# Kernel tuning notes

Measured on AMD Instinct MI355X. Metric: run time of the kernel, lower is better.

Reference implementation:

```python
import jax, jax.numpy as jnp
import numpy as np

L, T, B, D = 4, 512, 32, 1024
EPS = 1e-5


def _ln(x, g, b):
    # LayerNorm over last dim (torch nn.LayerNorm default eps=1e-5)
    m = jnp.mean(x, axis=-1, keepdims=True)
    v = jnp.var(x, axis=-1, keepdims=True)
    return (x - m) * jax.lax.rsqrt(v + EPS) * g + b


def setup_inputs() -> dict:
    key = jax.random.key(0)
    ks = jax.random.split(key, 6)
    s = np.float32(1.0 / np.sqrt(D))
    return {
        "x": jax.random.normal(ks[0], (T, B, D), dtype=jnp.float32),
        "state": jnp.zeros((L, B, D), dtype=jnp.float32),
        # per-layer gated-cell params (cell_cls(d_model, d_model))
        "Wf": jax.random.normal(ks[1], (L, D, D), dtype=jnp.float32) * s,
        "Uf": jax.random.normal(ks[2], (L, D, D), dtype=jnp.float32) * s,
        "bf": jnp.zeros((L, D), dtype=jnp.float32),
        "Wc": jax.random.normal(ks[3], (L, D, D), dtype=jnp.float32) * s,
        "Uc": jax.random.normal(ks[4], (L, D, D), dtype=jnp.float32) * s,
        "bc": jnp.zeros((L, D), dtype=jnp.float32),
        # per-layer pre-norm LayerNorm params
        "pre_gamma": jnp.ones((L, D), dtype=jnp.float32),
        "pre_beta": jnp.zeros((L, D), dtype=jnp.float32),
        # stack output norm params
        "stack_gamma": jnp.ones((D,), dtype=jnp.float32),
        "stack_beta": jnp.zeros((D,), dtype=jnp.float32),
    }


def reference(x, state, Wf, Uf, bf, Wc, Uc, bc, pre_gamma, pre_beta, stack_gamma, stack_beta):
    n_layers = state.shape[0]

    def step(states, xt):
        # states: [L, B, D]; xt: [B, D]
        h = xt
        new_states = []
        for i in range(n_layers):  # small fixed layer count
            hn = _ln(h, pre_gamma[i], pre_beta[i])
            si = states[i]
            fg = jax.nn.sigmoid(hn @ Wf[i] + si @ Uf[i] + bf[i])
            cand = jnp.tanh(hn @ Wc[i] + si @ Uc[i] + bc[i])
            ns = fg * si + (1.0 - fg) * cand
            new_states.append(ns)
            h = ns
        y_t = _ln(h, stack_gamma, stack_beta)
        return jnp.stack(new_states, axis=0), y_t

    new_state, y = jax.lax.scan(step, state, x)
    return y, new_state
```

## Files before the change

### kernel.cpp

```cpp
#include <hip/hip_runtime.h>
#include <cstdint>
#include <cstddef>

#define T_ 512
#define B_ 32
#define D_ 1024
#define L_ 4
#define BD_ (B_*D_)
#define TPB 256
#define NWG 256
#define EPSF 1e-5f

typedef _Float16 f16x8 __attribute__((ext_vector_type(8)));
typedef float f32x4 __attribute__((ext_vector_type(4)));
typedef float f32x2 __attribute__((ext_vector_type(2)));
typedef unsigned int u32x4 __attribute__((ext_vector_type(4)));
typedef unsigned long long u64;

#define WSO_PROG   0
#define WSO_WT     1048576
#define WSO_H16    34603008

#define LDS_W     0
#define LDS_DUMP  131072
#define LDS_GB    147456
#define LDS_NS    155904
#define LDS_BIAS  158464
#define LDS_SGSB  158592
#define LDS_RED   158720
#define LDS_TOTAL 160768
#define NSTR 20

__device__ __forceinline__ unsigned pk2h(float a, float b){
  _Float16 ha=(_Float16)a, hb=(_Float16)b;
  return (unsigned)__builtin_bit_cast(unsigned short,ha) |
         ((unsigned)__builtin_bit_cast(unsigned short,hb)<<16);
}
__device__ __forceinline__ unsigned cldu(const unsigned* p){
  return __hip_atomic_load(p,__ATOMIC_RELAXED,__HIP_MEMORY_SCOPE_AGENT);
}
__device__ __forceinline__ void cstore16(unsigned short* p, unsigned w0, unsigned w1, unsigned w2, unsigned w3){
  u64 lo=((u64)w1<<32)|w0, hi=((u64)w3<<32)|w2;
  __hip_atomic_store((u64*)(void*)p,     lo, __ATOMIC_RELAXED, __HIP_MEMORY_SCOPE_AGENT);
  __hip_atomic_store((u64*)(void*)(p+4), hi, __ATOMIC_RELAXED, __HIP_MEMORY_SCOPE_AGENT);
}

#define GLDX(d,vo,sb)  asm volatile("global_load_dwordx4 %0, %1, %2" : "=v"(d) : "v"(vo), "s"(sb) : "memory")
#define WAITV(N) do{ asm volatile("s_waitcnt vmcnt(" #N ")" ::: "memory"); __builtin_amdgcn_sched_barrier(0); }while(0)
#define BARS do{ asm volatile("s_waitcnt lgkmcnt(0)" ::: "memory"); __builtin_amdgcn_s_barrier(); }while(0)

#define MM(cc) do{ \
    const int kb_=(((cc)*128+kq))*2; \
    f16x8 bF=*(const f16x8*)(WF + (kb_^swl)); \
    f16x8 bC=*(const f16x8*)(WC + (kb_^swl)); \
    accF0=__builtin_amdgcn_mfma_f32_16x16x32_f16(a0,bF,accF0,0,0,0); \
    accF1=__builtin_amdgcn_mfma_f32_16x16x32_f16(a1,bF,accF1,0,0,0); \
    accC0=__builtin_amdgcn_mfma_f32_16x16x32_f16(a0,bC,accC0,0,0,0); \
    accC1=__builtin_amdgcn_mfma_f32_16x16x32_f16(a1,bC,accC1,0,0,0); \
  }while(0)

#define PSI(i,NW) do{ WAITV(NW); \
    f16x8 a0=__builtin_bit_cast(f16x8,pS[2*(i)]); \
    f16x8 a1=__builtin_bit_cast(f16x8,pS[2*(i)+1]); \
    MM(8+(i)); }while(0)

#define PHN(c) do{ \
    f16x8 a0=__builtin_bit_cast(f16x8,pH[2*(c)]); \
    f16x8 a1=__builtin_bit_cast(f16x8,pH[2*(c)+1]); \
    const int kf_=(c)*128+kq; \
    f16x8 g8=*(const f16x8*)(GBg16+(kf_>>1)); \
    f16x8 b8=*(const f16x8*)(GBg16+512+(kf_>>1)); \
    a0=a0*rsA8+nmA8; a0=a0*g8+b8; \
    a1=a1*rsB8+nmB8; a1=a1*g8+b8; \
    MM(c); }while(0)

#define PHX(c) do{ \
    f32x4 xa0=__builtin_bit_cast(f32x4,pX[4*(c)]),   xa1=__builtin_bit_cast(f32x4,pX[4*(c)+1]); \
    f32x4 xb0=__builtin_bit_cast(f32x4,pX[4*(c)+2]), xb1=__builtin_bit_cast(f32x4,pX[4*(c)+3]); \
    const int kf_=(c)*128+kq; \
    f32x4 g0=*(const f32x4*)(GBg32+kf_), g1=*(const f32x4*)(GBg32+kf_+4); \
    f32x4 q0=*(const f32x4*)(GBg32+1024+kf_), q1=*(const f32x4*)(GBg32+1024+kf_+4); \
    f16x8 a0,a1; \
    a0[0]=(_Float16)((xa0[0]*rsA+nmA)*g0[0]+q0[0]); a0[1]=(_Float16)((xa0[1]*rsA+nmA)*g0[1]+q0[1]); \
    a0[2]=(_Float16)((xa0[2]*rsA+nmA)*g0[2]+q0[2]); a0[3]=(_Float16)((xa0[3]*rsA+nmA)*g0[3]+q0[3]); \
    a0[4]=(_Float16)((xa1[0]*rsA+nmA)*g1[0]+q1[0]); a0[5]=(_Float16)((xa1[1]*rsA+nmA)*g1[1]+q1[1]); \
    a0[6]=(_Float16)((xa1[2]*rsA+nmA)*g1[2]+q1[2]); a0[7]=(_Float16)((xa1[3]*rsA+nmA)*g1[3]+q1[3]); \
    a1[0]=(_Float16)((xb0[0]*rsB+nmB)*g0[0]+q0[0]); a1[1]=(_Float16)((xb0[1]*rsB+nmB)*g0[1]+q0[1]); \
    a1[2]=(_Float16)((xb0[2]*rsB+nmB)*g0[2]+q0[2]); a1[3]=(_Float16)((xb0[3]*rsB+nmB)*g0[3]+q0[3]); \
    a1[4]=(_Float16)((xb1[0]*rsB+nmB)*g1[0]+q1[0]); a1[5]=(_Float16)((xb1[1]*rsB+nmB)*g1[1]+q1[1]); \
    a1[6]=(_Float16)((xb1[2]*rsB+nmB)*g1[2]+q1[2]); a1[7]=(_Float16)((xb1[3]*rsB+nmB)*g1[3]+q1[3]); \
    MM(c); }while(0)

extern "C" __global__ void __launch_bounds__(256,1) crs_prepass(
    const float* __restrict__ Wf, const float* __restrict__ Uf,
    const float* __restrict__ Wc, const float* __restrict__ Uc,
    unsigned short* __restrict__ WT)
{
  int bid = blockIdx.x;
  int kt  = bid & 15;
  int ct  = (bid>>4) & 31;
  int sel = (bid>>9) & 3;
  int i   = bid >> 11;
  int tid = threadIdx.x;
  int kq  = tid >> 5;
  int cc  = tid & 31;
  const float* sp;
  if      (sel==0) sp = Wf;
  else if (sel==1) sp = Uf;
  else if (sel==2) sp = Wc;
  else             sp = Uc;
  sp += (size_t)i * 1048576;
  int cl = ct*32 + cc;
  int k0 = kt*64 + kq*8;
  float f[8];
  #pragma unroll
  for (int e=0;e<8;++e){ f[e] = sp[(size_t)(k0+e)*1024 + cl]; }
  int cg = ((sel>>1) ? 1024 : 0) + cl;
  int ks = sel & 1;
  size_t idx = ((size_t)(i*2048 + cg)*2 + ks)*1024 + k0;
  uint4 pk;
  pk.x = pk2h(f[0], f[1]);
  pk.y = pk2h(f[2], f[3]);
  pk.z = pk2h(f[4], f[5]);
  pk.w = pk2h(f[6], f[7]);
  *(uint4*)(WT + idx) = pk;
}

extern "C" __global__ void __launch_bounds__(256,1) crs_prep2(
    const float* __restrict__ st0, unsigned short* __restrict__ H16)
{
  int i2=blockIdx.x, tid=threadIdx.x;
  int rr=tid>>3, ss=tid&7;
  const float4* p4=(const float4*)(st0+(size_t)i2*BD_+rr*1024+ss*128);
  uint4* dst=(uint4*)(H16+(size_t)i2*513*32768+rr*1024+ss*128);
  #pragma unroll
  for (int q=0;q<16;++q){
    float4 a=p4[2*q], b=p4[2*q+1];
    uint4 pk; pk.x=pk2h(a.x,a.y); pk.y=pk2h(a.z,a.w); pk.z=pk2h(b.x,b.y); pk.w=pk2h(b.z,b.w);
    dst[q]=pk;
  }
}

extern "C" __global__ void __launch_bounds__(TPB,1) crs_main(
    const float* __restrict__ x, const float* __restrict__ st0,
    const float* __restrict__ bfv, const float* __restrict__ bcv,
    const float* __restrict__ pg, const float* __restrict__ pb,
    const float* __restrict__ sg, const float* __restrict__ sbv,
    float* __restrict__ y, float* __restrict__ ostate,
    const unsigned short* __restrict__ WT, char* __restrict__ ws)
{
  extern __shared__ char smem[];
  const int tid=threadIdx.x, w=blockIdx.x;
  const int li=w>>6, wr=w&63;
  const int lane=tid&63, v=tid>>6;
  const int l15=lane&15, lg=(lane>>4)&3;
  const int kq = v*32 + lg*8;
  const int col=lane&15, rp=lane>>4;
  const int r0=v*8+rp, r1=v*8+4+rp;
  const int sseg=tid&7;

  unsigned* prog=(unsigned*)(ws+WSO_PROG);
  unsigned short* H16=(unsigned short*)(ws+WSO_H16);
  float* NSf=(float*)(smem+LDS_NS);
  float* BIAS=(float*)(smem+LDS_BIAS);
  float* SGSB=(float*)(smem+LDS_SGSB);
  char* RED0=smem+LDS_RED;
  char* RED1=smem+LDS_RED+1024;

  {
    int lc=tid>>3;
    int cgl=(lc>>4)*1024 + wr*16 + (lc&15);
    const unsigned short* src=WT + ((size_t)li*2048+cgl)*2048;
    char* dcol = smem + LDS_W + lc*4096;
    int sw2=(lc&7)<<4;
    #pragma unroll
    for (int n=0;n<32;++n){
      int q=sseg+n*8;
      uint4 d=*(const uint4*)(src+q*8);
      *(uint4*)(dcol + ((q*16)^sw2)) = d;
    }
  }
  if (li==0){
    float* g32=(float*)(smem+LDS_GB);
    for (int k=tid;k<1024;k+=TPB){ g32[k]=pg[k]; g32[1024+k]=pb[k]; }
  } else {
    unsigned* g16=(unsigned*)(smem+LDS_GB);
    for (int k=tid;k<512;k+=TPB){
      g16[k]    =pk2h(pg[li*1024+2*k], pg[li*1024+2*k+1]);
      g16[512+k]=pk2h(pb[li*1024+2*k], pb[li*1024+2*k+1]);
    }
  }
  if (tid<16) BIAS[tid]=bfv[li*1024+wr*16+tid];
  else if (tid<32) BIAS[tid]=bcv[li*1024+wr*16+(tid-16)];
  if (li==3){
    if (tid<16) SGSB[tid]=sg[wr*16+tid];
    else if (tid<32) SGSB[tid]=sbv[wr*16+(tid-16)];
  }
  f32x2 sreg, pns={0.f,0.f};
  sreg.x = st0[(size_t)li*BD_ + (size_t)r0*D_ + wr*16+col];
  sreg.y = st0[(size_t)li*BD_ + (size_t)r1*D_ + wr*16+col];
  __syncthreads();

  const char* WF = smem + LDS_W + l15*4096;
  const char* WC = smem + LDS_W + (16+l15)*4096;
  const int swl = (l15&7)<<4;
  const unsigned* GBg16 = (const unsigned*)(smem+LDS_GB);
  const float* GBg32 = (const float*)(smem+LDS_GB);
  const int voA = l15*2048 + kq*2, voB = voA + 32768;
  const int vxA = l15*4096 + kq*4, vxB = vxA + 65536;

  for (int t=0; t<T_; ++t){
    if (tid==0){
      const unsigned ow=64u*(unsigned)t;
      while (cldu(prog+li*64) < ow) __builtin_amdgcn_s_sleep(1);
    }
    __syncthreads();

    u64 sbS = (u64)(uintptr_t)(H16 + ((size_t)li*513 + (size_t)t)*32768);
    f32x4 accF0={0,0,0,0}, accF1={0,0,0,0}, accC0={0,0,0,0}, accC1={0,0,0,0};

    if (li==0){
      u64 sbH = (u64)(uintptr_t)(x + (size_t)t*BD_);
      u32x4 pS[16]; u32x4 pX[32];
      GLDX(pS[0],  voA+0*256, sbS); GLDX(pS[1],  voB+0*256, sbS);
      GLDX(pS[2],  voA+1*256, sbS); GLDX(pS[3],  voB+1*256, sbS);
      GLDX(pS[4],  voA+2*256, sbS); GLDX(pS[5],  voB+2*256, sbS);
      GLDX(pS[6],  voA+3*256, sbS); GLDX(pS[7],  voB+3*256, sbS);
      GLDX(pS[8],  voA+4*256, sbS); GLDX(pS[9],  voB+4*256, sbS);
      GLDX(pS[10], voA+5*256, sbS); GLDX(pS[11], voB+5*256, sbS);
      GLDX(pS[12], voA+6*256, sbS); GLDX(pS[13], voB+6*256, sbS);
      GLDX(pS[14], voA+7*256, sbS); GLDX(pS[15], voB+7*256, sbS);
      GLDX(pX[0],  vxA+0*512, sbH); GLDX(pX[1],  vxA+0*512+16, sbH); GLDX(pX[2],  vxB+0*512, sbH); GLDX(pX[3],  vxB+0*512+16, sbH);
      GLDX(pX[4],  vxA+1*512, sbH); GLDX(pX[5],  vxA+1*512+16, sbH); GLDX(pX[6],  vxB+1*512, sbH); GLDX(pX[7],  vxB+1*512+16, sbH);
      GLDX(pX[8],  vxA+2*512, sbH); GLDX(pX[9],  vxA+2*512+16, sbH); GLDX(pX[10], vxB+2*512, sbH); GLDX(pX[11], vxB+2*512+16, sbH);
      GLDX(pX[12], vxA+3*512, sbH); GLDX(pX[13], vxA+3*512+16, sbH); GLDX(pX[14], vxB+3*512, sbH); GLDX(pX[15], vxB+3*512+16, sbH);
      GLDX(pX[16], vxA+4*512, sbH); GLDX(pX[17], vxA+4*512+16, sbH); GLDX(pX[18], vxB+4*512, sbH); GLDX(pX[19], vxB+4*512+16, sbH);
      GLDX(pX[20], vxA+5*512, sbH); GLDX(pX[21], vxA+5*512+16, sbH); GLDX(pX[22], vxB+5*512, sbH); GLDX(pX[23], vxB+5*512+16, sbH);
      GLDX(pX[24], vxA+6*512, sbH); GLDX(pX[25], vxA+6*512+16, sbH); GLDX(pX[26], vxB+6*512, sbH); GLDX(pX[27], vxB+6*512+16, sbH);
      GLDX(pX[28], vxA+7*512, sbH); GLDX(pX[29], vxA+7*512+16, sbH); GLDX(pX[30], vxB+7*512, sbH); GLDX(pX[31], vxB+7*512+16, sbH);
      PSI(0,46); PSI(1,44); PSI(2,42); PSI(3,40); PSI(4,38); PSI(5,36); PSI(6,34); PSI(7,32);
      WAITV(0);
      float sA=0.f,qA=0.f,sB=0.f,qB=0.f;
      #pragma unroll
      for (int c2=0;c2<8;++c2){
        f32x4 u0=__builtin_bit_cast(f32x4,pX[4*c2]),   u1=__builtin_bit_cast(f32x4,pX[4*c2+1]);
        f32x4 w0=__builtin_bit_cast(f32x4,pX[4*c2+2]), w1=__builtin_bit_cast(f32x4,pX[4*c2+3]);
        #pragma unroll
        for (int j=0;j<4;++j){
          sA+=u0[j]; qA+=u0[j]*u0[j]; sA+=u1[j]; qA+=u1[j]*u1[j];
          sB+=w0[j]; qB+=w0[j]*w0[j]; sB+=w1[j]; qB+=w1[j]*w1[j];
        }
      }
      sA+=__shfl_xor(sA,16); qA+=__shfl_xor(qA,16); sB+=__shfl_xor(sB,16); qB+=__shfl_xor(qB,16);
      sA+=__shfl_xor(sA,32); qA+=__shfl_xor(qA,32); sB+=__shfl_xor(sB,32); qB+=__shfl_xor(qB,32);
      if (lane<16){ f32x4 pk={sA,qA,sB,qB}; *(f32x4*)(RED0+((v*16+lane)<<4))=pk; }
      BARS;
      f32x4 hp={0.f,0.f,0.f,0.f};
      #pragma unroll
      for (int vv=0;vv<4;++vv) hp += *(const f32x4*)(RED0+((vv*16+l15)<<4));
      float mA=hp.x*(1.f/1024.f);
      float rsA=rsqrtf(hp.y*(1.f/1024.f)-mA*mA+EPSF), nmA=-mA*rsA;
      float mB=hp.z*(1.f/1024.f);
      float rsB=rsqrtf(hp.w*(1.f/1024.f)-mB*mB+EPSF), nmB=-mB*rsB;
      PHX(0); PHX(1); PHX(2); PHX(3); PHX(4); PHX(5); PHX(6); PHX(7);
    } else {
      u64 sbH = (u64)(uintptr_t)(H16 + ((size_t)(li-1)*513 + (size_t)(t+1))*32768);
      u32x4 pS[16]; u32x4 pH[16];
      GLDX(pS[0],  voA+0*256, sbS); GLDX(pS[1],  voB+0*256, sbS);
      GLDX(pS[2],  voA+1*256, sbS); GLDX(pS[3],  voB+1*256, sbS);
      GLDX(pS[4],  voA+2*256, sbS); GLDX(pS[5],  voB+2*256, sbS);
      GLDX(pS[6],  voA+3*256, sbS); GLDX(pS[7],  voB+3*256, sbS);
      GLDX(pS[8],  voA+4*256, sbS); GLDX(pS[9],  voB+4*256, sbS);
      GLDX(pS[10], voA+5*256, sbS); GLDX(pS[11], voB+5*256, sbS);
      GLDX(pS[12], voA+6*256, sbS); GLDX(pS[13], voB+6*256, sbS);
      GLDX(pS[14], voA+7*256, sbS); GLDX(pS[15], voB+7*256, sbS);
      if (tid==0){
        const unsigned uw=64u*(unsigned)(t+1);
        while (cldu(prog+(li-1)*64) < uw) __builtin_amdgcn_s_sleep(1);
      }
      BARS;
      GLDX(pH[0],  voA+0*256, sbH); GLDX(pH[1],  voB+0*256, sbH);
      GLDX(pH[2],  voA+1*256, sbH); GLDX(pH[3],  voB+1*256, sbH);
      GLDX(pH[4],  voA+2*256, sbH); GLDX(pH[5],  voB+2*256, sbH);
      GLDX(pH[6],  voA+3*256, sbH); GLDX(pH[7],  voB+3*256, sbH);
      GLDX(pH[8],  voA+4*256, sbH); GLDX(pH[9],  voB+4*256, sbH);
      GLDX(pH[10], voA+5*256, sbH); GLDX(pH[11], voB+5*256, sbH);
      GLDX(pH[12], voA+6*256, sbH); GLDX(pH[13], voB+6*256, sbH);
      GLDX(pH[14], voA+7*256, sbH); GLDX(pH[15], voB+7*256, sbH);
      PSI(0,30); PSI(1,28); PSI(2,26); PSI(3,24); PSI(4,22); PSI(5,20); PSI(6,18); PSI(7,16);
      WAITV(0);
      float sA=0.f,qA=0.f,sB=0.f,qB=0.f;
      #pragma unroll
      for (int c2=0;c2<8;++c2){
        f16x8 hA=__builtin_bit_cast(f16x8,pH[2*c2]);
        f16x8 hB=__builtin_bit_cast(f16x8,pH[2*c2+1]);
        #pragma unroll
        for (int j=0;j<8;++j){
          float fa=(float)hA[j], fb=(float)hB[j];
          sA+=fa; qA+=fa*fa; sB+=fb; qB+=fb*fb;
        }
      }
      sA+=__shfl_xor(sA,16); qA+=__shfl_xor(qA,16); sB+=__shfl_xor(sB,16); qB+=__shfl_xor(qB,16);
      sA+=__shfl_xor(sA,32); qA+=__shfl_xor(qA,32); sB+=__shfl_xor(sB,32); qB+=__shfl_xor(qB,32);
      if (lane<16){ f32x4 pk={sA,qA,sB,qB}; *(f32x4*)(RED0+((v*16+lane)<<4))=pk; }
      if (li==3){
        float sS=0.f,qS=0.f,sT=0.f,qT=0.f;
        #pragma unroll
        for (int c2=0;c2<8;++c2){
          f16x8 tA=__builtin_bit_cast(f16x8,pS[2*c2]);
          f16x8 tB=__builtin_bit_cast(f16x8,pS[2*c2+1]);
          #pragma unroll
          for (int j=0;j<8;++j){
            float fa=(float)tA[j], fb=(float)tB[j];
            sS+=fa; qS+=fa*fa; sT+=fb; qT+=fb*fb;
          }
        }
        sS+=__shfl_xor(sS,16); qS+=__shfl_xor(qS,16); sT+=__shfl_xor(sT,16); qT+=__shfl_xor(qT,16);
        sS+=__shfl_xor(sS,32); qS+=__shfl_xor(qS,32); sT+=__shfl_xor(sT,32); qT+=__shfl_xor(qT,32);
        if (lane<16){ f32x4 pk={sS,qS,sT,qT}; *(f32x4*)(RED1+((v*16+lane)<<4))=pk; }
      }
      BARS;
      f32x4 hp={0.f,0.f,0.f,0.f};
      #pragma unroll
      for (int vv=0;vv<4;++vv) hp += *(const f32x4*)(RED0+((vv*16+l15)<<4));
      float mAf=hp.x*(1.f/1024.f);
      float rsAf=rsqrtf(hp.y*(1.f/1024.f)-mAf*mAf+EPSF), nmAf=-mAf*rsAf;
      float mBf=hp.z*(1.f/1024.f);
      float rsBf=rsqrtf(hp.w*(1.f/1024.f)-mBf*mBf+EPSF), nmBf=-mBf*rsBf;
      const _Float16 hrA=(_Float16)rsAf, hmA=(_Float16)nmAf, hrB=(_Float16)rsBf, hmB=(_Float16)nmBf;
      const f16x8 rsA8={hrA,hrA,hrA,hrA,hrA,hrA,hrA,hrA};
      const f16x8 nmA8={hmA,hmA,hmA,hmA,hmA,hmA,hmA,hmA};
      const f16x8 rsB8={hrB,hrB,hrB,hrB,hrB,hrB,hrB,hrB};
      const f16x8 nmB8={hmB,hmB,hmB,hmB,hmB,hmB,hmB,hmB};
      if (li==3 && t>=1){
        f32x4 sp0={0.f,0.f,0.f,0.f}, sp1={0.f,0.f,0.f,0.f};
        #pragma unroll
        for (int vv=0;vv<4;++vv){
          sp0 += *(const f32x4*)(RED1+((vv*16+(r0&15))<<4));
          sp1 += *(const f32x4*)(RED1+((vv*16+(r1&15))<<4));
        }
        float gv=SGSB[col], bv=SGSB[16+col];
        float s0=(r0<16)? sp0.x : sp0.z, q0=(r0<16)? sp0.y : sp0.w;
        float m0=s0*(1.f/1024.f);
        float rs0=rsqrtf(q0*(1.f/1024.f)-m0*m0+EPSF);
        y[(size_t)(t-1)*BD_+(size_t)r0*D_+wr*16+col]=(pns.x-m0)*rs0*gv+bv;
        float s1v=(r1<16)? sp1.x : sp1.z, q1v=(r1<16)? sp1.y : sp1.w;
        float m1=s1v*(1.f/1024.f);
        float rs1=rsqrtf(q1v*(1.f/1024.f)-m1*m1+EPSF);
        y[(size_t)(t-1)*BD_+(size_t)r1*D_+wr*16+col]=(pns.y-m1)*rs1*gv+bv;
      }
      PHN(0); PHN(1); PHN(2); PHN(3); PHN(4); PHN(5); PHN(6); PHN(7);
    }

    *(f32x4*)(smem+LDS_DUMP + (((v*4+0)*64+lane)<<4)) = accF0;
    *(f32x4*)(smem+LDS_DUMP + (((v*4+1)*64+lane)<<4)) = accF1;
    *(f32x4*)(smem+LDS_DUMP + (((v*4+2)*64+lane)<<4)) = accC0;
    *(f32x4*)(smem+LDS_DUMP + (((v*4+3)*64+lane)<<4)) = accC1;
    BARS;

    {
      const int rtl = v>>1;
      const int lg20 = (v&1)*2, lg21 = (v&1)*2+1;
      float fF0=0.f,fF1=0.f,fC0=0.f,fC1=0.f;
      #pragma unroll
      for (int v2=0;v2<4;++v2){
        const char* db = smem+LDS_DUMP + v2*4096;
        fF0 += *(const float*)(db + (((0+rtl)*64 + lg20*16+col)<<4) + rp*4);
        fF1 += *(const float*)(db + (((0+rtl)*64 + lg21*16+col)<<4) + rp*4);
        fC0 += *(const float*)(db + (((2+rtl)*64 + lg20*16+col)<<4) + rp*4);
        fC1 += *(const float*)(db + (((2+rtl)*64 + lg21*16+col)<<4) + rp*4);
      }
      float bfc=BIAS[col], bcc=BIAS[16+col];
      float preF0=fminf(fmaxf(fF0+bfc,-30.f),30.f);
      float preC0=fminf(fmaxf(fC0+bcc,-30.f),30.f);
      float preF1=fminf(fmaxf(fF1+bfc,-30.f),30.f);
      float preC1=fminf(fmaxf(fC1+bcc,-30.f),30.f);
      float fg0=1.f/(1.f+__expf(-preF0)), e0=__expf(-2.f*preC0);
      float cd0=(1.f-e0)/(1.f+e0);
      float fg1=1.f/(1.f+__expf(-preF1)), e1=__expf(-2.f*preC1);
      float cd1=(1.f-e1)/(1.f+e1);
      float ns0=fg0*sreg.x+(1.f-fg0)*cd0;
      float ns1=fg1*sreg.y+(1.f-fg1)*cd1;
      sreg.x=ns0; sreg.y=ns1;
      if (li==3){ pns.x=ns0; pns.y=ns1; }
      NSf[r0*NSTR+col]=ns0;
      NSf[r1*NSTR+col]=ns1;
    }
    BARS;

    if (lane<16){
      int row = v*8 + (lane>>1), hf = lane&1;
      const float* nr = NSf + row*NSTR + hf*8;
      f32x4 q0 = *(const f32x4*)nr, q1 = *(const f32x4*)(nr+4);
      unsigned w0=pk2h(q0[0],q0[1]), w1=pk2h(q0[2],q0[3]);
      unsigned w2=pk2h(q1[0],q1[1]), w3=pk2h(q1[2],q1[3]);
      unsigned short* sd = H16 + ((size_t)li*513 + (size_t)(t+1))*32768 + row*1024 + wr*16 + hf*8;
      cstore16(sd, w0, w1, w2, w3);
      if (t==T_-1){
        float* op = ostate + (size_t)li*BD_ + (size_t)row*D_ + wr*16 + hf*8;
        *(f32x4*)op = q0; *(f32x4*)(op+4) = q1;
      }
    }

    asm volatile("s_waitcnt vmcnt(0)" ::: "memory");
    __syncthreads();
    if (tid==0)
      __hip_atomic_fetch_add(prog+li*64, 1u, __ATOMIC_RELAXED, __HIP_MEMORY_SCOPE_AGENT);
  }

  if (li==3){
    if (tid==0){
      while (cldu(prog+3*64) < 64u*(unsigned)T_) __builtin_amdgcn_s_sleep(1);
    }
    __syncthreads();
    u64 sbS = (u64)(uintptr_t)(H16 + ((size_t)3*513 + (size_t)T_)*32768);
    u32x4 pS[16];
    GLDX(pS[0],  voA+0*256, sbS); GLDX(pS[1],  voB+0*256, sbS);
    GLDX(pS[2],  voA+1*256, sbS); GLDX(pS[3],  voB+1*256, sbS);
    GLDX(pS[4],  voA+2*256, sbS); GLDX(pS[5],  voB+2*256, sbS);
    GLDX(pS[6],  voA+3*256, sbS); GLDX(pS[7],  voB+3*256, sbS);
    GLDX(pS[8],  voA+4*256, sbS); GLDX(pS[9],  voB+4*256, sbS);
    GLDX(pS[10], voA+5*256, sbS); GLDX(pS[11], voB+5*256, sbS);
    GLDX(pS[12], voA+6*256, sbS); GLDX(pS[13], voB+6*256, sbS);
    GLDX(pS[14], voA+7*256, sbS); GLDX(pS[15], voB+7*256, sbS);
    WAITV(0);
    float sS=0.f,qS=0.f,sT=0.f,qT=0.f;
    #pragma unroll
    for (int c2=0;c2<8;++c2){
      f16x8 tA=__builtin_bit_cast(f16x8,pS[2*c2]);
      f16x8 tB=__builtin_bit_cast(f16x8,pS[2*c2+1]);
      #pragma unroll
      for (int j=0;j<8;++j){
        float fa=(float)tA[j], fb=(float)tB[j];
        sS+=fa; qS+=fa*fa; sT+=fb; qT+=fb*fb;
      }
    }
    sS+=__shfl_xor(sS,16); qS+=__shfl_xor(qS,16); sT+=__shfl_xor(sT,16); qT+=__shfl_xor(qT,16);
    sS+=__shfl_xor(sS,32); qS+=__shfl_xor(qS,32); sT+=__shfl_xor(sT,32); qT+=__shfl_xor(qT,32);
    if (lane<16){ f32x4 pk={sS,qS,sT,qT}; *(f32x4*)(RED1+((v*16+lane)<<4))=pk; }
    BARS;
    f32x4 sp0={0.f,0.f,0.f,0.f}, sp1={0.f,0.f,0.f,0.f};
    #pragma unroll
    for (int vv=0;vv<4;++vv){
      sp0 += *(const f32x4*)(RED1+((vv*16+(r0&15))<<4));
      sp1 += *(const f32x4*)(RED1+((vv*16+(r1&15))<<4));
    }
    float gv=SGSB[col], bv=SGSB[16+col];
    float s0=(r0<16)? sp0.x : sp0.z, q0=(r0<16)? sp0.y : sp0.w;
    float m0=s0*(1.f/1024.f);
    float rs0=rsqrtf(q0*(1.f/1024.f)-m0*m0+EPSF);
    y[(size_t)(T_-1)*BD_+(size_t)r0*D_+wr*16+col]=(pns.x-m0)*rs0*gv+bv;
    float s1v=(r1<16)? sp1.x : sp1.z, q1v=(r1<16)? sp1.y : sp1.w;
    float m1=s1v*(1.f/1024.f);
    float rs1=rsqrtf(q1v*(1.f/1024.f)-m1*m1+EPSF);
    y[(size_t)(T_-1)*BD_+(size_t)r1*D_+wr*16+col]=(pns.y-m1)*rs1*gv+bv;
  }
}

extern "C" void kernel_launch(void* const* d_in, const int* in_sizes, int n_in,
                              void* d_out, int out_size, void* d_ws, size_t ws_size,
                              hipStream_t stream){
  (void)in_sizes; (void)n_in; (void)out_size; (void)ws_size;
  const float* x   = (const float*)d_in[0];
  const float* st0 = (const float*)d_in[1];
  const float* Wf  = (const float*)d_in[2];
  const float* Uf  = (const float*)d_in[3];
  const float* bfv = (const float*)d_in[4];
  const float* Wc  = (const float*)d_in[5];
  const float* Uc  = (const float*)d_in[6];
  const float* bcv = (const float*)d_in[7];
  const float* pg  = (const float*)d_in[8];
  const float* pb  = (const float*)d_in[9];
  const float* sg  = (const float*)d_in[10];
  const float* sbv = (const float*)d_in[11];

  float* y      = (float*)d_out;
  float* ostate = y + (size_t)T_*BD_;
  char* ws = (char*)d_ws;

  (void)hipMemsetAsync(ws, 0, 4096, stream);
  hipLaunchKernelGGL(crs_prepass, dim3(8192), dim3(256), 0, stream,
                     Wf, Uf, Wc, Uc, (unsigned short*)(ws+WSO_WT));
  hipLaunchKernelGGL(crs_prep2, dim3(L_), dim3(256), 0, stream,
                     st0, (unsigned short*)(ws+WSO_H16));
  (void)hipFuncSetAttribute((const void*)crs_main, hipFuncAttributeMaxDynamicSharedMemorySize, LDS_TOTAL);
  hipLaunchKernelGGL(crs_main, dim3(NWG), dim3(TPB), LDS_TOTAL, stream,
                     x, st0, bfv, bcv, pg, pb, sg, sbv, y, ostate,
                     (const unsigned short*)(ws+WSO_WT), ws);
}
```

Before: 5.761 ms.

## Prefetch next-step layer input before state wait in recurrent persistent kernel

Moves the load of the next timestep's layer input (x for layer 0, the previous layer's h for the others) to the end of the current iteration, right after the progress counter is published. Its global-memory latency can then overlap the wait on this layer's own progress counter and the state load. It also swaps one block barrier before the fp16 store for an LDS-only wait and restructures the drain/barrier sequence. The cost is a long-lived 32-register prefetch buffer, which raises VGPR pressure, and reordered synchronisation that must stay correct across layers.

```diff
diff --git a/kernel.cpp b/kernel.cpp
--- a/kernel.cpp
+++ b/kernel.cpp
@@ -48,6 +48,8 @@
 #define GLDX(d,vo,sb)  asm volatile("global_load_dwordx4 %0, %1, %2" : "=v"(d) : "v"(vo), "s"(sb) : "memory")
 #define WAITV(N) do{ asm volatile("s_waitcnt vmcnt(" #N ")" ::: "memory"); __builtin_amdgcn_sched_barrier(0); }while(0)
 #define BARS do{ asm volatile("s_waitcnt lgkmcnt(0)" ::: "memory"); __builtin_amdgcn_s_barrier(); }while(0)
+#define WAITL do{ asm volatile("s_waitcnt lgkmcnt(0)" ::: "memory"); __builtin_amdgcn_sched_barrier(0); }while(0)
+#define DRAINV do{ asm volatile("s_waitcnt vmcnt(0)" ::: "memory"); __builtin_amdgcn_sched_barrier(0); }while(0)
 
 #define MM(cc) do{ \
     const int kb_=(((cc)*128+kq))*2; \
@@ -65,8 +67,8 @@
     MM(8+(i)); }while(0)
 
 #define PHN(c) do{ \
-    f16x8 a0=__builtin_bit_cast(f16x8,pH[2*(c)]); \
-    f16x8 a1=__builtin_bit_cast(f16x8,pH[2*(c)+1]); \
+    f16x8 a0=__builtin_bit_cast(f16x8,pP[2*(c)]); \
+    f16x8 a1=__builtin_bit_cast(f16x8,pP[2*(c)+1]); \
     const int kf_=(c)*128+kq; \
     f16x8 g8=*(const f16x8*)(GBg16+(kf_>>1)); \
     f16x8 b8=*(const f16x8*)(GBg16+512+(kf_>>1)); \
@@ -75,8 +77,8 @@
     MM(c); }while(0)
 
 #define PHX(c) do{ \
-    f32x4 xa0=__builtin_bit_cast(f32x4,pX[4*(c)]),   xa1=__builtin_bit_cast(f32x4,pX[4*(c)+1]); \
-    f32x4 xb0=__builtin_bit_cast(f32x4,pX[4*(c)+2]), xb1=__builtin_bit_cast(f32x4,pX[4*(c)+3]); \
+    f32x4 xa0=__builtin_bit_cast(f32x4,pP[4*(c)]),   xa1=__builtin_bit_cast(f32x4,pP[4*(c)+1]); \
+    f32x4 xb0=__builtin_bit_cast(f32x4,pP[4*(c)+2]), xb1=__builtin_bit_cast(f32x4,pP[4*(c)+3]); \
     const int kf_=(c)*128+kq; \
     f32x4 g0=*(const f32x4*)(GBg32+kf_), g1=*(const f32x4*)(GBg32+kf_+4); \
     f32x4 q0=*(const f32x4*)(GBg32+1024+kf_), q1=*(const f32x4*)(GBg32+1024+kf_+4); \
@@ -90,6 +92,39 @@
     a1[4]=(_Float16)((xb1[0]*rsB+nmB)*g1[0]+q1[0]); a1[5]=(_Float16)((xb1[1]*rsB+nmB)*g1[1]+q1[1]); \
     a1[6]=(_Float16)((xb1[2]*rsB+nmB)*g1[2]+q1[2]); a1[7]=(_Float16)((xb1[3]*rsB+nmB)*g1[3]+q1[3]); \
     MM(c); }while(0)
+
+#define LOAD_STATE(sb) do{ \
+  GLDX(pS[0],  voA+0*256, sb); GLDX(pS[1],  voB+0*256, sb); \
+  GLDX(pS[2],  voA+1*256, sb); GLDX(pS[3],  voB+1*256, sb); \
+  GLDX(pS[4],  voA+2*256, sb); GLDX(pS[5],  voB+2*256, sb); \
+  GLDX(pS[6],  voA+3*256, sb); GLDX(pS[7],  voB+3*256, sb); \
+  GLDX(pS[8],  voA+4*256, sb); GLDX(pS[9],  voB+4*256, sb); \
+  GLDX(pS[10], voA+5*256, sb); GLDX(pS[11], voB+5*256, sb); \
+  GLDX(pS[12], voA+6*256, sb); GLDX(pS[13], voB+6*256, sb); \
+  GLDX(pS[14], voA+7*256, sb); GLDX(pS[15], voB+7*256, sb); \
+}while(0)
+
+#define LOAD_H(sb) do{ \
+  GLDX(pP[0],  voA+0*256, sb); GLDX(pP[1],  voB+0*256, sb); \
+  GLDX(pP[2],  voA+1*256, sb); GLDX(pP[3],  voB+1*256, sb); \
+  GLDX(pP[4],  voA+2*256, sb); GLDX(pP[5],  voB+2*256, sb); \
+  GLDX(pP[6],  voA+3*256, sb); GLDX(pP[7],  voB+3*256, sb); \
+  GLDX(pP[8],  voA+4*256, sb); GLDX(pP[9],  voB+4*256, sb); \
+  GLDX(pP[10], voA+5*256, sb); GLDX(pP[11], voB+5*256, sb); \
+  GLDX(pP[12], voA+6*256, sb); GLDX(pP[13], voB+6*256, sb); \
+  GLDX(pP[14], voA+7*256, sb); GLDX(pP[15], voB+7*256, sb); \
+}while(0)
+
+#define LOAD_X(sb) do{ \
+  GLDX(pP[0],  vxA+0*512, sb); GLDX(pP[1],  vxA+0*512+16, sb); GLDX(pP[2],  vxB+0*512, sb); GLDX(pP[3],  vxB+0*512+16, sb); \
+  GLDX(pP[4],  vxA+1*512, sb); GLDX(pP[5],  vxA+1*512+16, sb); GLDX(pP[6],  vxB+1*512, sb); GLDX(pP[7],  vxB+1*512+16, sb); \
+  GLDX(pP[8],  vxA+2*512, sb); GLDX(pP[9],  vxA+2*512+16, sb); GLDX(pP[10], vxB+2*512, sb); GLDX(pP[11], vxB+2*512+16, sb); \
+  GLDX(pP[12], vxA+3*512, sb); GLDX(pP[13], vxA+3*512+16, sb); GLDX(pP[14], vxB+3*512, sb); GLDX(pP[15], vxB+3*512+16, sb); \
+  GLDX(pP[16], vxA+4*512, sb); GLDX(pP[17], vxA+4*512+16, sb); GLDX(pP[18], vxB+4*512, sb); GLDX(pP[19], vxB+4*512+16, sb); \
+  GLDX(pP[20], vxA+5*512, sb); GLDX(pP[21], vxA+5*512+16, sb); GLDX(pP[22], vxB+5*512, sb); GLDX(pP[23], vxB+5*512+16, sb); \
+  GLDX(pP[24], vxA+6*512, sb); GLDX(pP[25], vxA+6*512+16, sb); GLDX(pP[26], vxB+6*512, sb); GLDX(pP[27], vxB+6*512+16, sb); \
+  GLDX(pP[28], vxA+7*512, sb); GLDX(pP[29], vxA+7*512+16, sb); GLDX(pP[30], vxB+7*512, sb); GLDX(pP[31], vxB+7*512+16, sb); \
+}while(0)
 
 extern "C" __global__ void __launch_bounds__(256,1) crs_prepass(
     const float* __restrict__ Wf, const float* __restrict__ Uf,
@@ -209,42 +244,39 @@
   const int voA = l15*2048 + kq*2, voB = voA + 32768;
   const int vxA = l15*4096 + kq*4, vxB = vxA + 65536;
 
+  u32x4 pP[32];
+  u32x4 pS[16];
+
+  if (li==0){
+    u64 sbH=(u64)(uintptr_t)x;
+    LOAD_X(sbH);
+  } else {
+    if (tid==0){ while (cldu(prog+(li-1)*64) < 64u) __builtin_amdgcn_s_sleep(1); }
+    BARS;
+    u64 sbH=(u64)(uintptr_t)(H16 + ((size_t)(li-1)*513 + 1)*32768);
+    LOAD_H(sbH);
+  }
+
   for (int t=0; t<T_; ++t){
     if (tid==0){
       const unsigned ow=64u*(unsigned)t;
       while (cldu(prog+li*64) < ow) __builtin_amdgcn_s_sleep(1);
     }
-    __syncthreads();
+    BARS;
 
     u64 sbS = (u64)(uintptr_t)(H16 + ((size_t)li*513 + (size_t)t)*32768);
+    LOAD_STATE(sbS);
+
     f32x4 accF0={0,0,0,0}, accF1={0,0,0,0}, accC0={0,0,0,0}, accC1={0,0,0,0};
+    PSI(0,14); PSI(1,12); PSI(2,10); PSI(3,8); PSI(4,6); PSI(5,4); PSI(6,2); PSI(7,0);
+    WAITV(0);
 
     if (li==0){
-      u64 sbH = (u64)(uintptr_t)(x + (size_t)t*BD_);
-      u32x4 pS[16]; u32x4 pX[32];
-      GLDX(pS[0],  voA+0*256, sbS); GLDX(pS[1],  voB+0*256, sbS);
-      GLDX(pS[2],  voA+1*256, sbS); GLDX(pS[3],  voB+1*256, sbS);
-      GLDX(pS[4],  voA+2*256, sbS); GLDX(pS[5],  voB+2*256, sbS);
-      GLDX(pS[6],  voA+3*256, sbS); GLDX(pS[7],  voB+3*256, sbS);
-      GLDX(pS[8],  voA+4*256, sbS); GLDX(pS[9],  voB+4*256, sbS);
-      GLDX(pS[10], voA+5*256, sbS); GLDX(pS[11], voB+5*256, sbS);
-      GLDX(pS[12], voA+6*256, sbS); GLDX(pS[13], voB+6*256, sbS);
-      GLDX(pS[14], voA+7*256, sbS); GLDX(pS[15], voB+7*256, sbS);
-      GLDX(pX[0],  vxA+0*512, sbH); GLDX(pX[1],  vxA+0*512+16, sbH); GLDX(pX[2],  vxB+0*512, sbH); GLDX(pX[3],  vxB+0*512+16, sbH);
-      GLDX(pX[4],  vxA+1*512, sbH); GLDX(pX[5],  vxA+1*512+16, sbH); GLDX(pX[6],  vxB+1*512, sbH); GLDX(pX[7],  vxB+1*512+16, sbH);
-      GLDX(pX[8],  vxA+2*512, sbH); GLDX(pX[9],  vxA+2*512+16, sbH); GLDX(pX[10], vxB+2*512, sbH); GLDX(pX[11], vxB+2*512+16, sbH);
-      GLDX(pX[12], vxA+3*512, sbH); GLDX(pX[13], vxA+3*512+16, sbH); GLDX(pX[14], vxB+3*512, sbH); GLDX(pX[15], vxB+3*512+16, sbH);
-      GLDX(pX[16], vxA+4*512, sbH); GLDX(pX[17], vxA+4*512+16, sbH); GLDX(pX[18], vxB+4*512, sbH); GLDX(pX[19], vxB+4*512+16, sbH);
-      GLDX(pX[20], vxA+5*512, sbH); GLDX(pX[21], vxA+5*512+16, sbH); GLDX(pX[22], vxB+5*512, sbH); GLDX(pX[23], vxB+5*512+16, sbH);
-      GLDX(pX[24], vxA+6*512, sbH); GLDX(pX[25], vxA+6*512+16, sbH); GLDX(pX[26], vxB+6*512, sbH); GLDX(pX[27], vxB+6*512+16, sbH);
-      GLDX(pX[28], vxA+7*512, sbH); GLDX(pX[29], vxA+7*512+16, sbH); GLDX(pX[30], vxB+7*512, sbH); GLDX(pX[31], vxB+7*512+16, sbH);
-      PSI(0,46); PSI(1,44); PSI(2,42); PSI(3,40); PSI(4,38); PSI(5,36); PSI(6,34); PSI(7,32);
-      WAITV(0);
       float sA=0.f,qA=0.f,sB=0.f,qB=0.f;
       #pragma unroll
       for (int c2=0;c2<8;++c2){
-        f32x4 u0=__builtin_bit_cast(f32x4,pX[4*c2]),   u1=__builtin_bit_cast(f32x4,pX[4*c2+1]);
-        f32x4 w0=__builtin_bit_cast(f32x4,pX[4*c2+2]), w1=__builtin_bit_cast(f32x4,pX[4*c2+3]);
+        f32x4 u0=__builtin_bit_cast(f32x4,pP[4*c2]),   u1=__builtin_bit_cast(f32x4,pP[4*c2+1]);
+        f32x4 w0=__builtin_bit_cast(f32x4,pP[4*c2+2]), w1=__builtin_bit_cast(f32x4,pP[4*c2+3]);
         #pragma unroll
         for (int j=0;j<4;++j){
           sA+=u0[j]; qA+=u0[j]*u0[j]; sA+=u1[j]; qA+=u1[j]*u1[j];
@@ -264,36 +296,11 @@
       float rsB=rsqrtf(hp.w*(1.f/1024.f)-mB*mB+EPSF), nmB=-mB*rsB;
       PHX(0); PHX(1); PHX(2); PHX(3); PHX(4); PHX(5); PHX(6); PHX(7);
     } else {
-      u64 sbH = (u64)(uintptr_t)(H16 + ((size_t)(li-1)*513 + (size_t)(t+1))*32768);
-      u32x4 pS[16]; u32x4 pH[16];
-      GLDX(pS[0],  voA+0*256, sbS); GLDX(pS[1],  voB+0*256, sbS);
-      GLDX(pS[2],  voA+1*256, sbS); GLDX(pS[3],  voB+1*256, sbS);
-      GLDX(pS[4],  voA+2*256, sbS); GLDX(pS[5],  voB+2*256, sbS);
-      GLDX(pS[6],  voA+3*256, sbS); GLDX(pS[7],  voB+3*256, sbS);
-      GLDX(pS[8],  voA+4*256, sbS); GLDX(pS[9],  voB+4*256, sbS);
-      GLDX(pS[10], voA+5*256, sbS); GLDX(pS[11], voB+5*256, sbS);
-      GLDX(pS[12], voA+6*256, sbS); GLDX(pS[13], voB+6*256, sbS);
-      GLDX(pS[14], voA+7*256, sbS); GLDX(pS[15], voB+7*256, sbS);
-      if (tid==0){
-        const unsigned uw=64u*(unsigned)(t+1);
-        while (cldu(prog+(li-1)*64) < uw) __builtin_amdgcn_s_sleep(1);
-      }
-      BARS;
-      GLDX(pH[0],  voA+0*256, sbH); GLDX(pH[1],  voB+0*256, sbH);
-      GLDX(pH[2],  voA+1*256, sbH); GLDX(pH[3],  voB+1*256, sbH);
-      GLDX(pH[4],  voA+2*256, sbH); GLDX(pH[5],  voB+2*256, sbH);
-      GLDX(pH[6],  voA+3*256, sbH); GLDX(pH[7],  voB+3*256, sbH);
-      GLDX(pH[8],  voA+4*256, sbH); GLDX(pH[9],  voB+4*256, sbH);
-      GLDX(pH[10], voA+5*256, sbH); GLDX(pH[11], voB+5*256, sbH);
-      GLDX(pH[12], voA+6*256, sbH); GLDX(pH[13], voB+6*256, sbH);
-      GLDX(pH[14], voA+7*256, sbH); GLDX(pH[15], voB+7*256, sbH);
-      PSI(0,30); PSI(1,28); PSI(2,26); PSI(3,24); PSI(4,22); PSI(5,20); PSI(6,18); PSI(7,16);
-      WAITV(0);
       float sA=0.f,qA=0.f,sB=0.f,qB=0.f;
       #pragma unroll
       for (int c2=0;c2<8;++c2){
-        f16x8 hA=__builtin_bit_cast(f16x8,pH[2*c2]);
-        f16x8 hB=__builtin_bit_cast(f16x8,pH[2*c2+1]);
+        f16x8 hA=__builtin_bit_cast(f16x8,pP[2*c2]);
+        f16x8 hB=__builtin_bit_cast(f16x8,pP[2*c2+1]);
         #pragma unroll
         for (int j=0;j<8;++j){
           float fa=(float)hA[j], fb=(float)hB[j];
@@ -386,7 +393,7 @@
       NSf[r0*NSTR+col]=ns0;
       NSf[r1*NSTR+col]=ns1;
     }
-    BARS;
+    WAITL;
 
     if (lane<16){
       int row = v*8 + (lane>>1), hf = lane&1;
@@ -402,27 +409,34 @@
       }
     }
 
-    asm volatile("s_waitcnt vmcnt(0)" ::: "memory");
-    __syncthreads();
+    DRAINV;
+    BARS;
     if (tid==0)
       __hip_atomic_fetch_add(prog+li*64, 1u, __ATOMIC_RELAXED, __HIP_MEMORY_SCOPE_AGENT);
+
+    if (t+1 < T_){
+      if (li==0){
+        u64 sbH=(u64)(uintptr_t)(x + (size_t)(t+1)*BD_);
+        LOAD_X(sbH);
+      } else {
+        if (tid==0){
+          const unsigned uw=64u*(unsigned)(t+2);
+          while (cldu(prog+(li-1)*64) < uw) __builtin_amdgcn_s_sleep(1);
+        }
+        BARS;
+        u64 sbH=(u64)(uintptr_t)(H16 + ((size_t)(li-1)*513 + (size_t)(t+2))*32768);
+        LOAD_H(sbH);
+      }
+    }
   }
 
   if (li==3){
     if (tid==0){
       while (cldu(prog+3*64) < 64u*(unsigned)T_) __builtin_amdgcn_s_sleep(1);
     }
-    __syncthreads();
+    BARS;
     u64 sbS = (u64)(uintptr_t)(H16 + ((size_t)3*513 + (size_t)T_)*32768);
-    u32x4 pS[16];
-    GLDX(pS[0],  voA+0*256, sbS); GLDX(pS[1],  voB+0*256, sbS);
-    GLDX(pS[2],  voA+1*256, sbS); GLDX(pS[3],  voB+1*256, sbS);
-    GLDX(pS[4],  voA+2*256, sbS); GLDX(pS[5],  voB+2*256, sbS);
-    GLDX(pS[6],  voA+3*256, sbS); GLDX(pS[7],  voB+3*256, sbS);
-    GLDX(pS[8],  voA+4*256, sbS); GLDX(pS[9],  voB+4*256, sbS);
-    GLDX(pS[10], voA+5*256, sbS); GLDX(pS[11], voB+5*256, sbS);
-    GLDX(pS[12], voA+6*256, sbS); GLDX(pS[13], voB+6*256, sbS);
-    GLDX(pS[14], voA+7*256, sbS); GLDX(pS[15], voB+7*256, sbS);
+    LOAD_STATE(sbS);
     WAITV(0);
     float sS=0.f,qS=0.f,sT=0.f,qT=0.f;
     #pragma unroll
```

Measured after the change: 5.474 ms. 5.0% less time.
